# Performance work log

Measured on AMD Instinct MI355X. Metric: run time of the kernel, lower is better.

Reference implementation:

```python
import jax, jax.numpy as jnp
import numpy as np
from jax import lax

THETA = 1.0  # __init__ lengthscale arg
CLAMP_MIN = 1e-15


def setup_inputs() -> dict:
    key = jax.random.key(0)
    k1, k2 = jax.random.split(key)
    N, M, D = 8192, 8192, 64
    x1 = jax.random.normal(k1, (N, D), dtype=jnp.float32)
    x2 = jax.random.normal(k2, (M, D), dtype=jnp.float32)
    lengthscale = jnp.ones((1,), dtype=jnp.float32)  # nn.Parameter init to 1.0
    return {"x1": x1, "x2": x2, "lengthscale": lengthscale}


def _cdist_l1(a, b):
    # a: [N, D], b: [M, D] -> [N, M]; scan over feature dim to avoid
    # materializing an [N, M, D] broadcast intermediate.
    N, M = a.shape[0], b.shape[0]

    def step(acc, cols):
        ai, bi = cols  # [N], [M]
        return acc + jnp.abs(ai[:, None] - bi[None, :]), None

    acc0 = jnp.zeros((N, M), dtype=a.dtype)
    dist, _ = lax.scan(step, acc0, (a.T, b.T))
    return dist


def reference(x1, x2, lengthscale):
    # lengthscale per-dim vector = theta * learned scalar (broadcasts)
    ls = THETA * lengthscale[0]
    adjustment = jnp.mean(x1, axis=-2, keepdims=True)  # mean over x1 rows only
    x1_ = (x1 - adjustment) / ls
    x2_ = (x2 - adjustment) / ls
    distance = _cdist_l1(x1_, x2_)
    distance = jnp.maximum(distance, CLAMP_MIN)
    return jnp.exp(-distance)
```

## Files before the change

kernel.cpp:

```cpp
#include <hip/hip_runtime.h>
#include <math.h>

#define TILE 128
#define DDIM 64
#define NTH 256

__global__ void col_mean_kernel(const float* __restrict__ x1,
                                float* __restrict__ meanp, int N) {
  const int d = blockIdx.x;
  float s = 0.f;
  for (int i = threadIdx.x; i < N; i += NTH) {
    s += x1[(size_t)i * DDIM + d];
  }
  for (int off = 32; off > 0; off >>= 1) s += __shfl_down(s, off);
  __shared__ float part[NTH / 64];
  if ((threadIdx.x & 63) == 0) part[threadIdx.x >> 6] = s;
  __syncthreads();
  if (threadIdx.x == 0) {
    float t = 0.f;
    #pragma unroll
    for (int w = 0; w < NTH / 64; ++w) t += part[w];
    meanp[d] = t / (float)N;
  }
}

__global__ __launch_bounds__(NTH, 2) void laplace_tile_kernel(
    const float* __restrict__ x1, const float* __restrict__ x2,
    const float* __restrict__ lsp, const float* __restrict__ meanp,
    float* __restrict__ out, int N, int M) {
  __shared__ float at[TILE * DDIM];
  __shared__ float bt[TILE * DDIM];

  const int tid = threadIdx.x;
  const int ty = tid >> 4;
  const int tx = tid & 15;
  const int row0 = blockIdx.y * TILE;
  const int col0 = blockIdx.x * TILE;
  const float ls = lsp[0];

  {
    const int g = tid & 15;
    const int rb = tid >> 4;
    const float4 vm = *(const float4*)&meanp[g * 4];
    #pragma unroll
    for (int it = 0; it < 8; ++it) {
      const int r = it * 16 + rb;
      float4 va = *(const float4*)&x1[(size_t)(row0 + r) * DDIM + g * 4];
      float4 vb = *(const float4*)&x2[(size_t)(col0 + r) * DDIM + g * 4];
      va.x = (va.x - vm.x) / ls;  va.y = (va.y - vm.y) / ls;
      va.z = (va.z - vm.z) / ls;  va.w = (va.w - vm.w) / ls;
      vb.x = (vb.x - vm.x) / ls;  vb.y = (vb.y - vm.y) / ls;
      vb.z = (vb.z - vm.z) / ls;  vb.w = (vb.w - vm.w) / ls;
      const int swz = ((g ^ (r & 15)) << 2);
      *(float4*)&at[r * DDIM + swz] = va;
      *(float4*)&bt[r * DDIM + swz] = vb;
    }
  }
  __syncthreads();

  float acc[8][8];
  #pragma unroll
  for (int r = 0; r < 8; ++r)
    #pragma unroll
    for (int c = 0; c < 8; ++c) acc[r][c] = 0.f;

  for (int gg = 0; gg < 16; ++gg) {
    const int sa = ((gg ^ ty) << 2);
    const int sb = ((gg ^ tx) << 2);
    float4 a[8], b[8];
    #pragma unroll
    for (int r = 0; r < 8; ++r)
      a[r] = *(const float4*)&at[(16 * r + ty) * DDIM + sa];
    #pragma unroll
    for (int c = 0; c < 8; ++c)
      b[c] = *(const float4*)&bt[(16 * c + tx) * DDIM + sb];
    #pragma unroll
    for (int r = 0; r < 8; ++r) {
      #pragma unroll
      for (int c = 0; c < 8; ++c) {
        acc[r][c] += fabsf(a[r].x - b[c].x);
        acc[r][c] += fabsf(a[r].y - b[c].y);
        acc[r][c] += fabsf(a[r].z - b[c].z);
        acc[r][c] += fabsf(a[r].w - b[c].w);
      }
    }
  }

  const float CLAMP = 1e-15f;
  #pragma unroll
  for (int r = 0; r < 8; ++r) {
    const size_t orow = (size_t)(row0 + 16 * r + ty) * (size_t)M + col0 + tx;
    #pragma unroll
    for (int c = 0; c < 8; ++c) {
      out[orow + 16 * c] = expf(-fmaxf(acc[r][c], CLAMP));
    }
  }
}

extern "C" void kernel_launch(void* const* d_in, const int* in_sizes, int n_in,
                              void* d_out, int out_size, void* d_ws, size_t ws_size,
                              hipStream_t stream) {
  const float* x1 = (const float*)d_in[0];
  const float* x2 = (const float*)d_in[1];
  const float* ls = (const float*)d_in[2];
  float* out = (float*)d_out;
  float* meanp = (float*)d_ws;

  const int N = in_sizes[0] / DDIM;
  const int M = in_sizes[1] / DDIM;

  col_mean_kernel<<<DDIM, NTH, 0, stream>>>(x1, meanp, N);

  dim3 grid(M / TILE, N / TILE);
  laplace_tile_kernel<<<grid, NTH, 0, stream>>>(x1, x2, ls, meanp, out, N, M);
}
```

Baseline: 525.4 us.

## Parallelize column mean, restructure L1 inner loop, use fast exp

Replaces the column-mean kernel with a two-stage reduction: 64 blocks each write coalesced partial sums, and one final block combines them. The tile kernel now multiplies by a precomputed reciprocal of the lengthscale instead of dividing. Its inner loop loads one A float4 per row on the fly and uses a combined XOR swizzle for the B index, and it sums the four absolute differences as a pairwise tree before accumulating. The output uses __expf in place of expf, which is less accurate and adds one more kernel launch.

```diff
diff --git a/kernel.cpp b/kernel.cpp
--- a/kernel.cpp
+++ b/kernel.cpp
@@ -1,26 +1,45 @@
 #include <hip/hip_runtime.h>
 #include <math.h>
 
+#define DDIM 64
 #define TILE 128
-#define DDIM 64
 #define NTH 256
+#define MEAN_BLOCKS 64
 
-__global__ void col_mean_kernel(const float* __restrict__ x1,
-                                float* __restrict__ meanp, int N) {
-  const int d = blockIdx.x;
+__global__ void mean_partial_kernel(const float* __restrict__ x1,
+                                    float* __restrict__ partial, int N) {
+  const int rows_per_block = N / MEAN_BLOCKS;
+  const int r0 = blockIdx.x * rows_per_block;
+  const int t = threadIdx.x;
+  const int d = t & 63;
+  const int rsub = t >> 6;
   float s = 0.f;
-  for (int i = threadIdx.x; i < N; i += NTH) {
-    s += x1[(size_t)i * DDIM + d];
+  for (int it = 0; it < rows_per_block; it += 4) {
+    s += x1[(size_t)(r0 + it + rsub) * DDIM + d];
   }
-  for (int off = 32; off > 0; off >>= 1) s += __shfl_down(s, off);
-  __shared__ float part[NTH / 64];
-  if ((threadIdx.x & 63) == 0) part[threadIdx.x >> 6] = s;
+  __shared__ float part[4][DDIM];
+  part[rsub][d] = s;
   __syncthreads();
-  if (threadIdx.x == 0) {
-    float t = 0.f;
-    #pragma unroll
-    for (int w = 0; w < NTH / 64; ++w) t += part[w];
-    meanp[d] = t / (float)N;
+  if (t < DDIM) {
+    partial[blockIdx.x * DDIM + t] =
+        part[0][t] + part[1][t] + part[2][t] + part[3][t];
+  }
+}
+
+__global__ void mean_final_kernel(const float* __restrict__ partial,
+                                  float* __restrict__ meanp, int N) {
+  const int t = threadIdx.x;
+  const int d = t & 63;
+  const int chunk = t >> 6;
+  float s = 0.f;
+  for (int b = chunk * (MEAN_BLOCKS / 4); b < (chunk + 1) * (MEAN_BLOCKS / 4); ++b) {
+    s += partial[(size_t)b * DDIM + d];
+  }
+  __shared__ float part[4][DDIM];
+  part[chunk][d] = s;
+  __syncthreads();
+  if (t < DDIM) {
+    meanp[t] = (part[0][t] + part[1][t] + part[2][t] + part[3][t]) / (float)N;
   }
 }
 
@@ -36,7 +55,7 @@
   const int tx = tid & 15;
   const int row0 = blockIdx.y * TILE;
   const int col0 = blockIdx.x * TILE;
-  const float ls = lsp[0];
+  const float rls = 1.0f / lsp[0];
 
   {
     const int g = tid & 15;
@@ -47,10 +66,10 @@
       const int r = it * 16 + rb;
       float4 va = *(const float4*)&x1[(size_t)(row0 + r) * DDIM + g * 4];
       float4 vb = *(const float4*)&x2[(size_t)(col0 + r) * DDIM + g * 4];
-      va.x = (va.x - vm.x) / ls;  va.y = (va.y - vm.y) / ls;
-      va.z = (va.z - vm.z) / ls;  va.w = (va.w - vm.w) / ls;
-      vb.x = (vb.x - vm.x) / ls;  vb.y = (vb.y - vm.y) / ls;
-      vb.z = (vb.z - vm.z) / ls;  vb.w = (vb.w - vm.w) / ls;
+      va.x = (va.x - vm.x) * rls;  va.y = (va.y - vm.y) * rls;
+      va.z = (va.z - vm.z) * rls;  va.w = (va.w - vm.w) * rls;
+      vb.x = (vb.x - vm.x) * rls;  vb.y = (vb.y - vm.y) * rls;
+      vb.z = (vb.z - vm.z) * rls;  vb.w = (vb.w - vm.w) * rls;
       const int swz = ((g ^ (r & 15)) << 2);
       *(float4*)&at[r * DDIM + swz] = va;
       *(float4*)&bt[r * DDIM + swz] = vb;
@@ -58,41 +77,44 @@
   }
   __syncthreads();
 
+  const float4* at4 = (const float4*)at;
+  const float4* bt4 = (const float4*)bt;
+  int aoff[8], boff[8];
+  #pragma unroll
+  for (int r = 0; r < 8; ++r) aoff[r] = (16 * r + ty) * 16;
+  #pragma unroll
+  for (int c = 0; c < 8; ++c) boff[c] = (16 * c + tx) * 16;
+  const int kx = ty ^ tx;
+
   float acc[8][8];
   #pragma unroll
   for (int r = 0; r < 8; ++r)
     #pragma unroll
     for (int c = 0; c < 8; ++c) acc[r][c] = 0.f;
 
-  for (int gg = 0; gg < 16; ++gg) {
-    const int sa = ((gg ^ ty) << 2);
-    const int sb = ((gg ^ tx) << 2);
-    float4 a[8], b[8];
+  for (int gp = 0; gp < 16; ++gp) {
+    const int pb = gp ^ kx;
+    float4 b[8];
     #pragma unroll
-    for (int r = 0; r < 8; ++r)
-      a[r] = *(const float4*)&at[(16 * r + ty) * DDIM + sa];
-    #pragma unroll
-    for (int c = 0; c < 8; ++c)
-      b[c] = *(const float4*)&bt[(16 * c + tx) * DDIM + sb];
+    for (int c = 0; c < 8; ++c) b[c] = bt4[boff[c] + pb];
     #pragma unroll
     for (int r = 0; r < 8; ++r) {
+      const float4 a = at4[aoff[r] + gp];
       #pragma unroll
       for (int c = 0; c < 8; ++c) {
-        acc[r][c] += fabsf(a[r].x - b[c].x);
-        acc[r][c] += fabsf(a[r].y - b[c].y);
-        acc[r][c] += fabsf(a[r].z - b[c].z);
-        acc[r][c] += fabsf(a[r].w - b[c].w);
+        const float s01 = fabsf(a.x - b[c].x) + fabsf(a.y - b[c].y);
+        const float s23 = fabsf(a.z - b[c].z) + fabsf(a.w - b[c].w);
+        acc[r][c] += s01 + s23;
       }
     }
   }
 
-  const float CLAMP = 1e-15f;
   #pragma unroll
   for (int r = 0; r < 8; ++r) {
     const size_t orow = (size_t)(row0 + 16 * r + ty) * (size_t)M + col0 + tx;
     #pragma unroll
     for (int c = 0; c < 8; ++c) {
-      out[orow + 16 * c] = expf(-fmaxf(acc[r][c], CLAMP));
+      out[orow + 16 * c] = __expf(-fmaxf(acc[r][c], 1e-15f));
     }
   }
 }
@@ -105,11 +127,13 @@
   const float* ls = (const float*)d_in[2];
   float* out = (float*)d_out;
   float* meanp = (float*)d_ws;
+  float* partial = meanp + DDIM;
 
   const int N = in_sizes[0] / DDIM;
   const int M = in_sizes[1] / DDIM;
 
-  col_mean_kernel<<<DDIM, NTH, 0, stream>>>(x1, meanp, N);
+  mean_partial_kernel<<<MEAN_BLOCKS, NTH, 0, stream>>>(x1, partial, N);
+  mean_final_kernel<<<1, NTH, 0, stream>>>(partial, meanp, N);
 
   dim3 grid(M / TILE, N / TILE);
   laplace_tile_kernel<<<grid, NTH, 0, stream>>>(x1, x2, ls, meanp, out, N, M);
```

Measured after the change: 523.8 us. No clear change (-0.3%).
